# Optimization experiments

Hardware: AMD Instinct MI355X
Metric: run time of the kernel (lower is better)

The kernel has to match this reference:

```python
import jax, jax.numpy as jnp
import numpy as np

B, H, T, D = 4, 16, 2048, 64


def setup_inputs() -> dict:
    key = jax.random.key(0)
    kq, kk, kv = jax.random.split(key, 3)
    q = jax.random.normal(kq, (B, H, T, D), dtype=jnp.float32)
    k = jax.random.normal(kk, (B, H, T, D), dtype=jnp.float32)
    v = jax.random.normal(kv, (B, H, T, D), dtype=jnp.float32)
    return {"q": q, "k": k, "v": v}


def reference(q, k, v):
    # scores: [B,H,T,T] = q @ k^T (no softmax, linear attention)
    scores = jnp.einsum("bhtd,bhsd->bhts", q, k)
    # causal multiplicative mask: lower-triangular ones (zero out future keys)
    t = q.shape[-2]
    causal = jnp.tril(jnp.ones((t, t), dtype=scores.dtype))  # [T,T]
    scores = scores * causal  # broadcast over [B,H]
    # output: [B,H,T,D] = masked_scores @ v
    return jnp.einsum("bhts,bhsd->bhtd", scores, v)
```

## Files before the change

kernel.cpp:

```cpp
#include <hip/hip_runtime.h>
#include <hip/hip_bf16.h>


#define B_   4
#define H_   16
#define T_   2048
#define D_   64
#define BH_  64
#define CCH  256
#define NCH  8
#define LPAD 8
#define LW   (D_ + LPAD)

typedef __bf16 bf16x8 __attribute__((ext_vector_type(8)));
typedef float  f32x4  __attribute__((ext_vector_type(4)));


__global__ __launch_bounds__(256) void kv_chunk_kernel(
    const float* __restrict__ k, const float* __restrict__ v,
    float* __restrict__ kvws) {
  __shared__ __align__(16) __bf16 KT[D_][LW];
  __shared__ __align__(16) __bf16 VT[D_][LW];

  const int tid  = threadIdx.x;
  const int lane = tid & 63;
  const int w    = tid >> 6;
  const int quad = lane >> 4;
  const int l15  = lane & 15;
  const int bh   = blockIdx.x >> 3;
  const int c    = blockIdx.x & (NCH - 1);
  const long base = ((long)bh * T_ + (long)c * CCH) * D_;

  const f32x4 vzero = {0.f, 0.f, 0.f, 0.f};
  f32x4 acc[4];
#pragma unroll
  for (int n = 0; n < 4; ++n) acc[n] = vzero;

  const int sl = tid >> 2;
  const int d0 = (tid & 3) * 16;

  for (int st = 0; st < 4; ++st) {
    __syncthreads();
    {
      const float* krow = k + base + (long)(st * 64 + sl) * D_ + d0;
      const float* vrow = v + base + (long)(st * 64 + sl) * D_ + d0;
#pragma unroll
      for (int x4 = 0; x4 < 4; ++x4) {
        float4 kx = *(const float4*)(krow + x4 * 4);
        float4 vx = *(const float4*)(vrow + x4 * 4);
        int dd = d0 + x4 * 4;
        KT[dd + 0][sl] = (__bf16)kx.x;
        KT[dd + 1][sl] = (__bf16)kx.y;
        KT[dd + 2][sl] = (__bf16)kx.z;
        KT[dd + 3][sl] = (__bf16)kx.w;
        VT[dd + 0][sl] = (__bf16)vx.x;
        VT[dd + 1][sl] = (__bf16)vx.y;
        VT[dd + 2][sl] = (__bf16)vx.z;
        VT[dd + 3][sl] = (__bf16)vx.w;
      }
    }
    __syncthreads();
#pragma unroll
    for (int ks = 0; ks < 2; ++ks) {
      bf16x8 a = *(const bf16x8*)&KT[w * 16 + l15][ks * 32 + quad * 8];
#pragma unroll
      for (int n = 0; n < 4; ++n) {
        bf16x8 b = *(const bf16x8*)&VT[n * 16 + l15][ks * 32 + quad * 8];
        acc[n] = __builtin_amdgcn_mfma_f32_16x16x32_bf16(a, b, acc[n], 0, 0, 0);
      }
    }
  }
  float* out = kvws + ((long)blockIdx.x << 12);
#pragma unroll
  for (int n = 0; n < 4; ++n)
#pragma unroll
    for (int rr = 0; rr < 4; ++rr)
      out[(w * 16 + quad * 4 + rr) * 64 + n * 16 + l15] = acc[n][rr];
}

__global__ __launch_bounds__(256) void attn_chunk_kernel(
    const float* __restrict__ q, const float* __restrict__ k,
    const float* __restrict__ v, const float* __restrict__ kvws,
    float* __restrict__ out) {
  __shared__ __align__(16) __bf16 KVT[D_][LW];
  __shared__ __align__(16) __bf16 Kj[64][LW];
  __shared__ __align__(16) __bf16 VTj[D_][LW];
  __shared__ __align__(16) __bf16 Sw[4][16][LW];

  const int tid  = threadIdx.x;
  const int lane = tid & 63;
  const int w    = tid >> 6;
  const int quad = lane >> 4;
  const int l15  = lane & 15;
  const int bh   = blockIdx.x >> 3;
  const int c    = blockIdx.x & (NCH - 1);
  const long base = ((long)bh * T_ + (long)c * CCH) * D_;

  float kvacc[16];
#pragma unroll
  for (int i = 0; i < 16; ++i) kvacc[i] = 0.f;
  const float* wsbh = kvws + ((long)(bh * NCH) << 12);
  for (int cc = 0; cc < c; ++cc) {
    const float* p = wsbh + ((long)cc << 12) + tid;
#pragma unroll
    for (int i = 0; i < 16; ++i) kvacc[i] += p[i << 8];
  }
#pragma unroll
  for (int i = 0; i < 16; ++i) {
    int lin = tid + (i << 8);
    int d1 = lin >> 6, d2 = lin & 63;
    KVT[d2][d1] = (__bf16)kvacc[i];
  }

  bf16x8 qf[4][2];
#pragma unroll
  for (int i = 0; i < 4; ++i) {
    int row = (w + 4 * i) * 16 + l15;
    const float* qp = q + base + (long)row * D_ + quad * 8;
#pragma unroll
    for (int ks = 0; ks < 2; ++ks) {
      float4 lo = *(const float4*)(qp + ks * 32);
      float4 hi = *(const float4*)(qp + ks * 32 + 4);
      bf16x8 f;
      f[0] = (__bf16)lo.x; f[1] = (__bf16)lo.y;
      f[2] = (__bf16)lo.z; f[3] = (__bf16)lo.w;
      f[4] = (__bf16)hi.x; f[5] = (__bf16)hi.y;
      f[6] = (__bf16)hi.z; f[7] = (__bf16)hi.w;
      qf[i][ks] = f;
    }
  }

  const f32x4 vzero = {0.f, 0.f, 0.f, 0.f};
  f32x4 acc[4][4];
#pragma unroll
  for (int i = 0; i < 4; ++i)
#pragma unroll
    for (int n = 0; n < 4; ++n) acc[i][n] = vzero;

  __syncthreads();

#pragma unroll
  for (int ks = 0; ks < 2; ++ks)
#pragma unroll
    for (int n = 0; n < 4; ++n) {
      bf16x8 b = *(const bf16x8*)&KVT[n * 16 + l15][ks * 32 + quad * 8];
#pragma unroll
      for (int i = 0; i < 4; ++i)
        acc[i][n] =
            __builtin_amdgcn_mfma_f32_16x16x32_bf16(qf[i][ks], b, acc[i][n], 0, 0, 0);
    }

  const int sl = tid >> 2;
  const int d0 = (tid & 3) * 16;
  for (int j = 0; j < 4; ++j) {
    __syncthreads();
    {
      const float* krow = k + base + (long)(j * 64 + sl) * D_ + d0;
      const float* vrow = v + base + (long)(j * 64 + sl) * D_ + d0;
#pragma unroll
      for (int x4 = 0; x4 < 4; ++x4) {
        float4 kx = *(const float4*)(krow + x4 * 4);
        float4 vx = *(const float4*)(vrow + x4 * 4);
        int dd = d0 + x4 * 4;
        Kj[sl][dd + 0] = (__bf16)kx.x;
        Kj[sl][dd + 1] = (__bf16)kx.y;
        Kj[sl][dd + 2] = (__bf16)kx.z;
        Kj[sl][dd + 3] = (__bf16)kx.w;
        VTj[dd + 0][sl] = (__bf16)vx.x;
        VTj[dd + 1][sl] = (__bf16)vx.y;
        VTj[dd + 2][sl] = (__bf16)vx.z;
        VTj[dd + 3][sl] = (__bf16)vx.w;
      }
    }
    __syncthreads();
    for (int i = j; i < 4; ++i) {
      f32x4 s[4];
#pragma unroll
      for (int n = 0; n < 4; ++n) s[n] = vzero;
#pragma unroll
      for (int ks = 0; ks < 2; ++ks) {
#pragma unroll
        for (int n = 0; n < 4; ++n) {
          bf16x8 b = *(const bf16x8*)&Kj[n * 16 + l15][ks * 32 + quad * 8];
          s[n] = __builtin_amdgcn_mfma_f32_16x16x32_bf16(qf[i][ks], b, s[n], 0, 0, 0);
        }
      }
      __syncthreads();
#pragma unroll
      for (int n = 0; n < 4; ++n) {
#pragma unroll
        for (int rr = 0; rr < 4; ++rr) {
          float val = s[n][rr];
          if (i == j) {
            if (n * 16 + l15 > 16 * w + quad * 4 + rr) val = 0.f;
          }
          Sw[w][quad * 4 + rr][n * 16 + l15] = (__bf16)val;
        }
      }
      __syncthreads();
#pragma unroll
      for (int ks = 0; ks < 2; ++ks) {
        bf16x8 a = *(const bf16x8*)&Sw[w][l15][ks * 32 + quad * 8];
#pragma unroll
        for (int n = 0; n < 4; ++n) {
          bf16x8 b = *(const bf16x8*)&VTj[n * 16 + l15][ks * 32 + quad * 8];
          acc[i][n] =
              __builtin_amdgcn_mfma_f32_16x16x32_bf16(a, b, acc[i][n], 0, 0, 0);
        }
      }
    }
  }

  float* op = out + base;
#pragma unroll
  for (int i = 0; i < 4; ++i) {
    int row = (w + 4 * i) * 16 + quad * 4;
#pragma unroll
    for (int n = 0; n < 4; ++n)
#pragma unroll
      for (int rr = 0; rr < 4; ++rr)
        op[(long)(row + rr) * D_ + n * 16 + l15] = acc[i][n][rr];
  }
}

extern "C" void kernel_launch(void* const* d_in, const int* in_sizes, int n_in,
                              void* d_out, int out_size, void* d_ws, size_t ws_size,
                              hipStream_t stream) {
  const float* q = (const float*)d_in[0];
  const float* k = (const float*)d_in[1];
  const float* v = (const float*)d_in[2];
  float* out = (float*)d_out;
  float* kvws = (float*)d_ws;

  hipLaunchKernelGGL(kv_chunk_kernel, dim3(BH_ * NCH), dim3(256), 0, stream,
                     k, v, kvws);
  hipLaunchKernelGGL(attn_chunk_kernel, dim3(BH_ * NCH), dim3(256), 0, stream,
                     q, k, v, kvws, out);
}
```

Before: 150.9 us.

## Double-buffer K/V staging, vectorize LDS writes, drop per-tile block barriers

Both kernels now double-buffer the K/V shared-memory tiles, prefetching the next tile into registers while the MFMAs on the current tile run. The staging writes use vectorized bf16x4/bf16x8 stores in place of scalar transposed stores. In the attention kernel, the K and V fragments are hoisted into registers once per tile. The S tile is computed transposed (K as the A operand), so each wave writes its own Sw slice with packed stores, and the two __syncthreads per inner iteration are removed, relying on wave-private Sw. This adds register pressure, as hinted by launch_bounds(256,2), and risks an LDS hazard if wave-local ordering of the Sw write and read is not guaranteed.

After: 143.7 us. 4.8% less time.

```diff
diff --git a/kernel.cpp b/kernel.cpp
--- a/kernel.cpp
+++ b/kernel.cpp
@@ -12,15 +12,16 @@
 #define LPAD 8
 #define LW   (D_ + LPAD)
 
+typedef __bf16 bf16x4 __attribute__((ext_vector_type(4)));
 typedef __bf16 bf16x8 __attribute__((ext_vector_type(8)));
 typedef float  f32x4  __attribute__((ext_vector_type(4)));
 
 
-__global__ __launch_bounds__(256) void kv_chunk_kernel(
+__global__ __launch_bounds__(256, 2) void kv_chunk_kernel(
     const float* __restrict__ k, const float* __restrict__ v,
     float* __restrict__ kvws) {
-  __shared__ __align__(16) __bf16 KT[D_][LW];
-  __shared__ __align__(16) __bf16 VT[D_][LW];
+  __shared__ __align__(16) __bf16 KT[2][D_][LW];
+  __shared__ __align__(16) __bf16 VT[2][D_][LW];
 
   const int tid  = threadIdx.x;
   const int lane = tid & 63;
@@ -31,43 +32,57 @@
   const int c    = blockIdx.x & (NCH - 1);
   const long base = ((long)bh * T_ + (long)c * CCH) * D_;
 
+  const int s4 = tid >> 4;
+  const int d4 = tid & 15;
+
+  f32x4 kreg[4], vreg[4];
+  const float* kp0 = k + base + (long)(s4 * 4) * D_ + d4 * 4;
+  const float* vp0 = v + base + (long)(s4 * 4) * D_ + d4 * 4;
+
+  auto LOAD = [&](int st) {
+#pragma unroll
+    for (int r = 0; r < 4; ++r) {
+      kreg[r] = *(const f32x4*)(kp0 + (long)(st * 64 + r) * D_);
+      vreg[r] = *(const f32x4*)(vp0 + (long)(st * 64 + r) * D_);
+    }
+  };
+  auto WRITE = [&](int p) {
+#pragma unroll
+    for (int cc2 = 0; cc2 < 4; ++cc2) {
+      bf16x4 ka, va;
+#pragma unroll
+      for (int r = 0; r < 4; ++r) {
+        ka[r] = (__bf16)kreg[r][cc2];
+        va[r] = (__bf16)vreg[r][cc2];
+      }
+      *(bf16x4*)&KT[p][d4 * 4 + cc2][s4 * 4] = ka;
+      *(bf16x4*)&VT[p][d4 * 4 + cc2][s4 * 4] = va;
+    }
+  };
+
   const f32x4 vzero = {0.f, 0.f, 0.f, 0.f};
   f32x4 acc[4];
 #pragma unroll
   for (int n = 0; n < 4; ++n) acc[n] = vzero;
 
-  const int sl = tid >> 2;
-  const int d0 = (tid & 3) * 16;
-
+  LOAD(0);
+  WRITE(0);
+  __syncthreads();
   for (int st = 0; st < 4; ++st) {
-    __syncthreads();
-    {
-      const float* krow = k + base + (long)(st * 64 + sl) * D_ + d0;
-      const float* vrow = v + base + (long)(st * 64 + sl) * D_ + d0;
-#pragma unroll
-      for (int x4 = 0; x4 < 4; ++x4) {
-        float4 kx = *(const float4*)(krow + x4 * 4);
-        float4 vx = *(const float4*)(vrow + x4 * 4);
-        int dd = d0 + x4 * 4;
-        KT[dd + 0][sl] = (__bf16)kx.x;
-        KT[dd + 1][sl] = (__bf16)kx.y;
-        KT[dd + 2][sl] = (__bf16)kx.z;
-        KT[dd + 3][sl] = (__bf16)kx.w;
-        VT[dd + 0][sl] = (__bf16)vx.x;
-        VT[dd + 1][sl] = (__bf16)vx.y;
-        VT[dd + 2][sl] = (__bf16)vx.z;
-        VT[dd + 3][sl] = (__bf16)vx.w;
-      }
-    }
-    __syncthreads();
+    const int p = st & 1;
+    if (st < 3) LOAD(st + 1);
 #pragma unroll
     for (int ks = 0; ks < 2; ++ks) {
-      bf16x8 a = *(const bf16x8*)&KT[w * 16 + l15][ks * 32 + quad * 8];
+      bf16x8 a = *(const bf16x8*)&KT[p][w * 16 + l15][ks * 32 + quad * 8];
 #pragma unroll
       for (int n = 0; n < 4; ++n) {
-        bf16x8 b = *(const bf16x8*)&VT[n * 16 + l15][ks * 32 + quad * 8];
+        bf16x8 b = *(const bf16x8*)&VT[p][n * 16 + l15][ks * 32 + quad * 8];
         acc[n] = __builtin_amdgcn_mfma_f32_16x16x32_bf16(a, b, acc[n], 0, 0, 0);
       }
+    }
+    if (st < 3) {
+      WRITE(p ^ 1);
+      __syncthreads();
     }
   }
   float* out = kvws + ((long)blockIdx.x << 12);
@@ -78,13 +93,13 @@
       out[(w * 16 + quad * 4 + rr) * 64 + n * 16 + l15] = acc[n][rr];
 }
 
-__global__ __launch_bounds__(256) void attn_chunk_kernel(
+__global__ __launch_bounds__(256, 2) void attn_chunk_kernel(
     const float* __restrict__ q, const float* __restrict__ k,
     const float* __restrict__ v, const float* __restrict__ kvws,
     float* __restrict__ out) {
   __shared__ __align__(16) __bf16 KVT[D_][LW];
-  __shared__ __align__(16) __bf16 Kj[64][LW];
-  __shared__ __align__(16) __bf16 VTj[D_][LW];
+  __shared__ __align__(16) __bf16 Kj[2][64][LW];
+  __shared__ __align__(16) __bf16 VTj[2][D_][LW];
   __shared__ __align__(16) __bf16 Sw[4][16][LW];
 
   const int tid  = threadIdx.x;
@@ -96,20 +111,58 @@
   const int c    = blockIdx.x & (NCH - 1);
   const long base = ((long)bh * T_ + (long)c * CCH) * D_;
 
+  const int slK = tid >> 2;
+  const int d0K = (tid & 3) * 16;
+  const int s4  = tid >> 4;
+  const int d4  = tid & 15;
+
+  f32x4 kreg[4], vreg[4];
+  auto LOADJ = [&](int j) {
+    const float* kp = k + base + (long)(j * 64 + slK) * D_ + d0K;
+    const float* vp = v + base + (long)(j * 64 + s4 * 4) * D_ + d4 * 4;
+#pragma unroll
+    for (int r = 0; r < 4; ++r) kreg[r] = *(const f32x4*)(kp + r * 4);
+#pragma unroll
+    for (int r = 0; r < 4; ++r) vreg[r] = *(const f32x4*)(vp + (long)r * D_);
+  };
+  auto WRITEJ = [&](int p) {
+    bf16x8 kb0, kb1;
+#pragma unroll
+    for (int e = 0; e < 4; ++e) {
+      kb0[e]     = (__bf16)kreg[0][e];
+      kb0[4 + e] = (__bf16)kreg[1][e];
+      kb1[e]     = (__bf16)kreg[2][e];
+      kb1[4 + e] = (__bf16)kreg[3][e];
+    }
+    *(bf16x8*)&Kj[p][slK][d0K]     = kb0;
+    *(bf16x8*)&Kj[p][slK][d0K + 8] = kb1;
+#pragma unroll
+    for (int cc2 = 0; cc2 < 4; ++cc2) {
+      bf16x4 va;
+#pragma unroll
+      for (int r = 0; r < 4; ++r) va[r] = (__bf16)vreg[r][cc2];
+      *(bf16x4*)&VTj[p][d4 * 4 + cc2][s4 * 4] = va;
+    }
+  };
+
   float kvacc[16];
 #pragma unroll
   for (int i = 0; i < 16; ++i) kvacc[i] = 0.f;
   const float* wsbh = kvws + ((long)(bh * NCH) << 12);
   for (int cc = 0; cc < c; ++cc) {
-    const float* p = wsbh + ((long)cc << 12) + tid;
-#pragma unroll
-    for (int i = 0; i < 16; ++i) kvacc[i] += p[i << 8];
-  }
-#pragma unroll
-  for (int i = 0; i < 16; ++i) {
-    int lin = tid + (i << 8);
-    int d1 = lin >> 6, d2 = lin & 63;
-    KVT[d2][d1] = (__bf16)kvacc[i];
+    const float* pp = wsbh + ((long)cc << 12) + tid * 16;
+#pragma unroll
+    for (int x = 0; x < 4; ++x) {
+      f32x4 t = *(const f32x4*)(pp + x * 4);
+#pragma unroll
+      for (int e = 0; e < 4; ++e) kvacc[x * 4 + e] += t[e];
+    }
+  }
+  {
+    const int d1  = tid >> 2;
+    const int d2b = (tid & 3) * 16;
+#pragma unroll
+    for (int ii = 0; ii < 16; ++ii) KVT[d2b + ii][d1] = (__bf16)kvacc[ii];
   }
 
   bf16x8 qf[4][2];
@@ -119,13 +172,14 @@
     const float* qp = q + base + (long)row * D_ + quad * 8;
 #pragma unroll
     for (int ks = 0; ks < 2; ++ks) {
-      float4 lo = *(const float4*)(qp + ks * 32);
-      float4 hi = *(const float4*)(qp + ks * 32 + 4);
+      f32x4 lo = *(const f32x4*)(qp + ks * 32);
+      f32x4 hi = *(const f32x4*)(qp + ks * 32 + 4);
       bf16x8 f;
-      f[0] = (__bf16)lo.x; f[1] = (__bf16)lo.y;
-      f[2] = (__bf16)lo.z; f[3] = (__bf16)lo.w;
-      f[4] = (__bf16)hi.x; f[5] = (__bf16)hi.y;
-      f[6] = (__bf16)hi.z; f[7] = (__bf16)hi.w;
+#pragma unroll
+      for (int e = 0; e < 4; ++e) {
+        f[e]     = (__bf16)lo[e];
+        f[4 + e] = (__bf16)hi[e];
+      }
       qf[i][ks] = f;
     }
   }
@@ -137,7 +191,10 @@
 #pragma unroll
     for (int n = 0; n < 4; ++n) acc[i][n] = vzero;
 
+  LOADJ(0);
+  WRITEJ(0);
   __syncthreads();
+  LOADJ(1);
 
 #pragma unroll
   for (int ks = 0; ks < 2; ++ks)
@@ -150,64 +207,50 @@
             __builtin_amdgcn_mfma_f32_16x16x32_bf16(qf[i][ks], b, acc[i][n], 0, 0, 0);
     }
 
-  const int sl = tid >> 2;
-  const int d0 = (tid & 3) * 16;
   for (int j = 0; j < 4; ++j) {
-    __syncthreads();
-    {
-      const float* krow = k + base + (long)(j * 64 + sl) * D_ + d0;
-      const float* vrow = v + base + (long)(j * 64 + sl) * D_ + d0;
-#pragma unroll
-      for (int x4 = 0; x4 < 4; ++x4) {
-        float4 kx = *(const float4*)(krow + x4 * 4);
-        float4 vx = *(const float4*)(vrow + x4 * 4);
-        int dd = d0 + x4 * 4;
-        Kj[sl][dd + 0] = (__bf16)kx.x;
-        Kj[sl][dd + 1] = (__bf16)kx.y;
-        Kj[sl][dd + 2] = (__bf16)kx.z;
-        Kj[sl][dd + 3] = (__bf16)kx.w;
-        VTj[dd + 0][sl] = (__bf16)vx.x;
-        VTj[dd + 1][sl] = (__bf16)vx.y;
-        VTj[dd + 2][sl] = (__bf16)vx.z;
-        VTj[dd + 3][sl] = (__bf16)vx.w;
-      }
-    }
-    __syncthreads();
+    const int p = j & 1;
+    bf16x8 kfrag[2][4], vfrag[2][4];
+#pragma unroll
+    for (int ks = 0; ks < 2; ++ks)
+#pragma unroll
+      for (int n = 0; n < 4; ++n) {
+        kfrag[ks][n] = *(const bf16x8*)&Kj[p][n * 16 + l15][ks * 32 + quad * 8];
+        vfrag[ks][n] = *(const bf16x8*)&VTj[p][n * 16 + l15][ks * 32 + quad * 8];
+      }
     for (int i = j; i < 4; ++i) {
       f32x4 s[4];
 #pragma unroll
       for (int n = 0; n < 4; ++n) s[n] = vzero;
 #pragma unroll
-      for (int ks = 0; ks < 2; ++ks) {
-#pragma unroll
-        for (int n = 0; n < 4; ++n) {
-          bf16x8 b = *(const bf16x8*)&Kj[n * 16 + l15][ks * 32 + quad * 8];
-          s[n] = __builtin_amdgcn_mfma_f32_16x16x32_bf16(qf[i][ks], b, s[n], 0, 0, 0);
-        }
-      }
-      __syncthreads();
+      for (int ks = 0; ks < 2; ++ks)
+#pragma unroll
+        for (int n = 0; n < 4; ++n)
+          s[n] = __builtin_amdgcn_mfma_f32_16x16x32_bf16(kfrag[ks][n], qf[i][ks],
+                                                         s[n], 0, 0, 0);
 #pragma unroll
       for (int n = 0; n < 4; ++n) {
+        bf16x4 pk;
 #pragma unroll
         for (int rr = 0; rr < 4; ++rr) {
           float val = s[n][rr];
-          if (i == j) {
-            if (n * 16 + l15 > 16 * w + quad * 4 + rr) val = 0.f;
-          }
-          Sw[w][quad * 4 + rr][n * 16 + l15] = (__bf16)val;
+          if (i == j && (n * 16 + quad * 4 + rr > 16 * w + l15)) val = 0.f;
+          pk[rr] = (__bf16)val;
         }
-      }
-      __syncthreads();
+        *(bf16x4*)&Sw[w][l15][n * 16 + quad * 4] = pk;
+      }
 #pragma unroll
       for (int ks = 0; ks < 2; ++ks) {
         bf16x8 a = *(const bf16x8*)&Sw[w][l15][ks * 32 + quad * 8];
 #pragma unroll
-        for (int n = 0; n < 4; ++n) {
-          bf16x8 b = *(const bf16x8*)&VTj[n * 16 + l15][ks * 32 + quad * 8];
+        for (int n = 0; n < 4; ++n)
           acc[i][n] =
-              __builtin_amdgcn_mfma_f32_16x16x32_bf16(a, b, acc[i][n], 0, 0, 0);
-        }
-      }
+              __builtin_amdgcn_mfma_f32_16x16x32_bf16(a, vfrag[ks][n], acc[i][n], 0, 0, 0);
+      }
+    }
+    if (j < 3) {
+      WRITEJ(p ^ 1);
+      __syncthreads();
+      if (j < 2) LOADJ(j + 2);
     }
   }
 
```
